# Optimization experiments

Measured on AMD Instinct MI355X. Metric: run time of the kernel, lower is better.

## Reference

```python
import jax, jax.numpy as jnp
import numpy as np

BS, NC, CN, DN = 8, 1024, 64, 64
GH, GW = 32, 32
ALPHA, BPC = 4, 4
G = 8
IN_LO, IN_HI = 0, ALPHA
OUT_LO, OUT_HI = ALPHA, 2 * ALPHA
B_LO, B_HI = 2 * ALPHA, 2 * ALPHA + BPC
HS, HM, HMOD = 256, 256, 128
MOD_IN = 3 * DN + 2 + BPC
MOD_OUT = DN + BPC


def setup_inputs():
    key = jax.random.key(0)
    ks = iter(jax.random.split(key, 40))
    def nrm(shape, s=0.05):
        return jax.random.normal(next(ks), shape, dtype=jnp.float32) * s
    return {
        "x": nrm((BS, NC * DN), 1.0),
        "h": nrm((BS, NC, CN, DN), 0.01),
        "msg": nrm((BS, NC, CN, DN), 0.1),
        "W": nrm((BS, NC, CN, CN), 0.1),
        "decay_logit": jnp.zeros((BS, NC, CN), jnp.float32),
        "cell_context": jnp.zeros((BS, NC, DN), jnp.float32),
        "border_gate_logit": jnp.zeros((BS, NC, BPC), jnp.float32),
        "neuron_id": nrm((NC, CN, DN), 0.02),
        "state_w1": nrm((HS, 2 * DN)), "state_b1": jnp.zeros((HS,), jnp.float32),
        "state_gs1": jnp.ones((G, HS), jnp.float32), "state_gb1": jnp.zeros((G, HS), jnp.float32),
        "state_w2": nrm((DN, HS)), "state_b2": jnp.zeros((DN,), jnp.float32),
        "state_gs2": jnp.ones((G, DN), jnp.float32), "state_gb2": jnp.zeros((G, DN), jnp.float32),
        "msg_w1": nrm((HM, DN)), "msg_b1": jnp.zeros((HM,), jnp.float32),
        "msg_gs1": jnp.ones((G, HM), jnp.float32), "msg_gb1": jnp.zeros((G, HM), jnp.float32),
        "msg_w2": nrm((DN, HM)), "msg_b2": jnp.zeros((DN,), jnp.float32),
        "msg_gs2": jnp.ones((G, DN), jnp.float32), "msg_gb2": jnp.zeros((G, DN), jnp.float32),
        "inject_w": nrm((G, ALPHA * DN, DN)), "inject_b": jnp.zeros((G, ALPHA * DN), jnp.float32),
        "mod_w1": nrm((NC, MOD_IN, HMOD)), "mod_b1": jnp.zeros((NC, HMOD), jnp.float32),
        "mod_w2": nrm((NC, HMOD, MOD_OUT), 0.01), "mod_b2": jnp.zeros((NC, MOD_OUT), jnp.float32),
        "cell_to_group": jnp.arange(NC, dtype=jnp.int32) % G,
    }


def _grouped_mlp(x, c2g, w1, b1, gs1, gb1, w2, b2, gs2, gb2):
    # x: [B, NC, CN, F]; group-specific affine modulation after each linear.
    hid = jnp.einsum('bcnf,hf->bcnh', x, w1) + b1
    hid = jnp.tanh(hid * gs1[c2g][None, :, None, :] + gb1[c2g][None, :, None, :])
    out = jnp.einsum('bcnh,dh->bcnd', hid, w2) + b2
    return jnp.tanh(out * gs2[c2g][None, :, None, :] + gb2[c2g][None, :, None, :])


def reference(x, h, msg, W, decay_logit, cell_context, border_gate_logit, neuron_id,
              state_w1, state_b1, state_gs1, state_gb1, state_w2, state_b2, state_gs2, state_gb2,
              msg_w1, msg_b1, msg_gs1, msg_gb1, msg_w2, msg_b2, msg_gs2, msg_gb2,
              inject_w, inject_b, mod_w1, mod_b1, mod_w2, mod_b2, cell_to_group):
    c2g = cell_to_group
    # 1) dense message passing inside each cell: received = W @ msg
    received = jnp.einsum('bcnm,bcmd->bcnd', W, msg)
    # 2) inject external input into input ports (per-group orthogonal-init projections)
    cell_slice = x.reshape(BS, NC, DN)
    iw, ib = inject_w[c2g], inject_b[c2g]                      # [NC, alpha*DN, DN], [NC, alpha*DN]
    inject = jnp.einsum('bni,noi->bno', cell_slice, iw) + ib   # [BS, NC, alpha*DN]
    received = received.at[:, :, IN_LO:IN_HI].add(inject.reshape(BS, NC, ALPHA, DN))
    # 3) fixed geometric border exchange between neighboring grid cells
    border = msg[:, :, B_LO:B_HI].reshape(BS, GH, GW, BPC, DN)
    incoming = jnp.zeros_like(border)
    incoming = incoming.at[:, 1:, :, 0].set(border[:, :-1, :, 1])
    incoming = incoming.at[:, :-1, :, 1].set(border[:, 1:, :, 0])
    incoming = incoming.at[:, :, 1:, 2].set(border[:, :, :-1, 3])
    incoming = incoming.at[:, :, :-1, 3].set(border[:, :, 1:, 2])
    incoming = incoming.reshape(BS, NC, BPC, DN)
    border_gate = jax.nn.sigmoid(border_gate_logit)[..., None]
    received = received.at[:, :, B_LO:B_HI].add(border_gate * incoming)
    # 4) gated recurrent state update
    decay = jax.nn.sigmoid(decay_logit)[..., None]
    cand = _grouped_mlp(jnp.concatenate([received, h], axis=-1), c2g,
                        state_w1, state_b1, state_gs1, state_gb1,
                        state_w2, state_b2, state_gs2, state_gb2)
    h_new = decay * h + (1.0 - decay) * cand
    # 5) emit new messages (+ per-neuron identity embedding)
    msg_new = _grouped_mlp(h_new, c2g, msg_w1, msg_b1, msg_gs1, msg_gb1,
                           msg_w2, msg_b2, msg_gs2, msg_gb2) + neuron_id[None]
    # 6) readout from output ports
    readout = (msg_new[:, :, OUT_LO:OUT_HI].sum(axis=2) * (ALPHA ** -0.5)).reshape(BS, -1)
    # 7) per-cell modulation MLP (distinct weights per cell)
    h_mean = h_new.mean(axis=2)
    msg_mean = msg_new.mean(axis=2)
    W_row = jnp.abs(W).mean(axis=-1).mean(axis=2, keepdims=True)
    decay_mean = decay_logit.mean(axis=2, keepdims=True)
    feats = jnp.concatenate([h_mean, msg_mean, W_row, decay_mean,
                             cell_context, border_gate_logit], axis=-1)   # [BS, NC, MOD_IN]
    hid = jnp.tanh(jnp.einsum('bcf,cfh->bch', feats, mod_w1) + mod_b1)
    mod = jnp.einsum('bch,cho->bco', hid, mod_w2) + mod_b2                 # [BS, NC, MOD_OUT]
    cell_context_new = cell_context + mod[..., :DN]
    border_gate_logit_new = border_gate_logit + mod[..., DN:]
    return readout, h_new, msg_new, cell_context_new, border_gate_logit_new
```

## Files before the change

### kernel.cpp

```cpp
#include <hip/hip_runtime.h>

#define NCC 1024
#define MODIN 198
#define MODOUT 68
#define HMODL 128

typedef __attribute__((ext_vector_type(8))) short s8v;
typedef __attribute__((ext_vector_type(4))) float f4v;
typedef unsigned short ushort_t;
typedef unsigned int uint_t;

#define OFF_SW1 0
#define OFF_SW2 32768
#define OFF_MW1 49152
#define OFF_MW2 65536
#define FEATS_BYTE_OFF 262144

__device__ __forceinline__ float fast_tanh(float x) {
    const float e = __builtin_amdgcn_exp2f(x * 2.885390081777927f);
    const float r = __builtin_amdgcn_rcpf(e + 1.f);
    return fmaf(-2.f, r, 1.f);
}
__device__ __forceinline__ float fast_sigmoid(float x) {
    const float e = __builtin_amdgcn_exp2f(x * -1.4426950408889634f);
    return __builtin_amdgcn_rcpf(e + 1.f);
}
__device__ __forceinline__ ushort_t f2bf(float x) {
    uint_t u = __builtin_bit_cast(uint_t, x);
    u += 0x7FFFu + ((u >> 16) & 1u);
    return (ushort_t)(u >> 16);
}
__device__ __forceinline__ uint_t pk2(float a, float b) {
    uint_t r;
    asm("v_cvt_pk_bf16_f32 %0, %1, %2" : "=v"(r) : "v"(a), "v"(b));
    return r;
}
#define SWZ(byteoff, row) ((byteoff) ^ (((row) & 7) << 4))

__global__ __launch_bounds__(256)
void mg_cvtw(const float* __restrict__ sw1, const float* __restrict__ sw2,
             const float* __restrict__ mw1, const float* __restrict__ mw2,
             ushort_t* __restrict__ o) {
    const int i = blockIdx.x * 256 + threadIdx.x;
    float v;
    if (i < 32768)      v = sw1[i];
    else if (i < 49152) v = sw2[i - 32768];
    else if (i < 65536) v = mw1[i - 49152];
    else                v = mw2[i - 65536];
    o[i] = f2bf(v);
}

__global__ __launch_bounds__(256, 4)
void mg_inject(const float* __restrict__ xp, const float* __restrict__ iw,
               const float* __restrict__ ibias, const int* __restrict__ c2g,
               float* __restrict__ injb) {
    const int c = blockIdx.x, t = threadIdx.x;
    const int g = c2g[c];
    __shared__ float s_x[8][64];
    for (int idx = t; idx < 512; idx += 256)
        s_x[idx >> 6][idx & 63] = xp[(size_t)(idx >> 6) * (NCC * 64) + c * 64 + (idx & 63)];
    __syncthreads();
    const float* wrow = iw + (size_t)g * 16384 + t * 64;
    float a0 = 0.f, a1 = 0.f, a2 = 0.f, a3 = 0.f, a4 = 0.f, a5 = 0.f, a6 = 0.f, a7 = 0.f;
    #pragma unroll
    for (int i = 0; i < 64; i += 4) {
        const float4 w4 = *(const float4*)(wrow + i);
        const float4 x0 = *(const float4*)&s_x[0][i];
        const float4 x1 = *(const float4*)&s_x[1][i];
        const float4 x2 = *(const float4*)&s_x[2][i];
        const float4 x3 = *(const float4*)&s_x[3][i];
        const float4 x4 = *(const float4*)&s_x[4][i];
        const float4 x5 = *(const float4*)&s_x[5][i];
        const float4 x6 = *(const float4*)&s_x[6][i];
        const float4 x7 = *(const float4*)&s_x[7][i];
        a0 = fmaf(w4.x, x0.x, a0); a0 = fmaf(w4.y, x0.y, a0); a0 = fmaf(w4.z, x0.z, a0); a0 = fmaf(w4.w, x0.w, a0);
        a1 = fmaf(w4.x, x1.x, a1); a1 = fmaf(w4.y, x1.y, a1); a1 = fmaf(w4.z, x1.z, a1); a1 = fmaf(w4.w, x1.w, a1);
        a2 = fmaf(w4.x, x2.x, a2); a2 = fmaf(w4.y, x2.y, a2); a2 = fmaf(w4.z, x2.z, a2); a2 = fmaf(w4.w, x2.w, a2);
        a3 = fmaf(w4.x, x3.x, a3); a3 = fmaf(w4.y, x3.y, a3); a3 = fmaf(w4.z, x3.z, a3); a3 = fmaf(w4.w, x3.w, a3);
        a4 = fmaf(w4.x, x4.x, a4); a4 = fmaf(w4.y, x4.y, a4); a4 = fmaf(w4.z, x4.z, a4); a4 = fmaf(w4.w, x4.w, a4);
        a5 = fmaf(w4.x, x5.x, a5); a5 = fmaf(w4.y, x5.y, a5); a5 = fmaf(w4.z, x5.z, a5); a5 = fmaf(w4.w, x5.w, a5);
        a6 = fmaf(w4.x, x6.x, a6); a6 = fmaf(w4.y, x6.y, a6); a6 = fmaf(w4.z, x6.z, a6); a6 = fmaf(w4.w, x6.w, a6);
        a7 = fmaf(w4.x, x7.x, a7); a7 = fmaf(w4.y, x7.y, a7); a7 = fmaf(w4.z, x7.z, a7); a7 = fmaf(w4.w, x7.w, a7);
    }
    const float bv = ibias[g * 256 + t];
    const float acc[8] = {a0, a1, a2, a3, a4, a5, a6, a7};
    #pragma unroll
    for (int b = 0; b < 8; b++)
        injb[((size_t)b * NCC + c) * 4096 + t] = acc[b] + bv;
}

__global__ __launch_bounds__(512, 4)
void mg_cell_kernel(
    const float* __restrict__ hp,   const float* __restrict__ msgp,
    const float* __restrict__ Wp,   const float* __restrict__ decayp,
    const float* __restrict__ bglp, const float* __restrict__ nidp,
    const float* __restrict__ sb1,  const float* __restrict__ sgs1,
    const float* __restrict__ sgb1, const float* __restrict__ sb2,
    const float* __restrict__ sgs2, const float* __restrict__ sgb2,
    const float* __restrict__ mb1,  const float* __restrict__ mgs1,
    const float* __restrict__ mgb1, const float* __restrict__ mb2,
    const float* __restrict__ mgs2, const float* __restrict__ mgb2,
    const int*   __restrict__ c2g,  const ushort_t* __restrict__ wb,
    float* __restrict__ out_read, float* __restrict__ out_h,
    float* __restrict__ out_msg,  float* __restrict__ wsf)
{
    const int t  = threadIdx.x;
    const int bc = blockIdx.x;
    const int b  = bc >> 10, c = bc & 1023;
    const int gh = c >> 5, gwc = c & 31;
    const int lane = t & 63, w = t >> 6;
    const int cl = lane & 15, q = lane >> 4;
    const int g  = c2g[c];
    const size_t tile = (size_t)bc * 4096;

    __shared__ ushort_t sHid[8192];
    __shared__ ushort_t sIn[8192];
    __shared__ float s_scr[256];
    __shared__ float s_dec[64];
    __shared__ float s_wsum[8];
    __shared__ float s_dsum;

    ushort_t* sW    = sHid;
    ushort_t* sMsgT = sHid + 4096;

    {
        const int n = t >> 3, m0 = (t & 7) * 8;
        const float* src = Wp + tile + n * 64 + m0;
        const float4 v0 = *(const float4*)(src);
        const float4 v1 = *(const float4*)(src + 4);
        float wsum = fabsf(v0.x) + fabsf(v0.y) + fabsf(v0.z) + fabsf(v0.w)
                   + fabsf(v1.x) + fabsf(v1.y) + fabsf(v1.z) + fabsf(v1.w);
        *(uint_t*)((char*)sW + SWZ(n * 128 + (m0 + 0) * 2, n)) = pk2(v0.x, v0.y);
        *(uint_t*)((char*)sW + SWZ(n * 128 + (m0 + 2) * 2, n)) = pk2(v0.z, v0.w);
        *(uint_t*)((char*)sW + SWZ(n * 128 + (m0 + 4) * 2, n)) = pk2(v1.x, v1.y);
        *(uint_t*)((char*)sW + SWZ(n * 128 + (m0 + 6) * 2, n)) = pk2(v1.z, v1.w);
        #pragma unroll
        for (int off = 32; off > 0; off >>= 1) wsum += __shfl_down(wsum, off);
        if (lane == 0) s_wsum[w] = wsum;
    }
    #pragma unroll
    for (int i = 0; i < 2; i++) {
        const int m = (t >> 4) + i * 32, d0 = (t & 15) * 4;
        const float4 v = *(const float4*)(msgp + tile + (size_t)m * 64 + d0);
        *(ushort_t*)((char*)sMsgT + SWZ((d0 + 0) * 128 + m * 2, d0 + 0)) = f2bf(v.x);
        *(ushort_t*)((char*)sMsgT + SWZ((d0 + 1) * 128 + m * 2, d0 + 1)) = f2bf(v.y);
        *(ushort_t*)((char*)sMsgT + SWZ((d0 + 2) * 128 + m * 2, d0 + 2)) = f2bf(v.z);
        *(ushort_t*)((char*)sMsgT + SWZ((d0 + 3) * 128 + m * 2, d0 + 3)) = f2bf(v.w);
    }
    #pragma unroll
    for (int i = 0; i < 2; i++) {
        const int n = (t >> 4) + i * 32, d0 = (t & 15) * 4;
        const float4 v = *(const float4*)(hp + tile + (size_t)n * 64 + d0);
        *(uint_t*)((char*)sIn + SWZ(n * 256 + (64 + d0) * 2, n))     = pk2(v.x, v.y);
        *(uint_t*)((char*)sIn + SWZ(n * 256 + (64 + d0 + 2) * 2, n)) = pk2(v.z, v.w);
    }
    if (t < 256) {
        const int p = w, dd = lane;
        int ok, nc2, qq;
        if      (p == 0) { ok = (gh > 0);   nc2 = c - 32; qq = 1; }
        else if (p == 1) { ok = (gh < 31);  nc2 = c + 32; qq = 0; }
        else if (p == 2) { ok = (gwc > 0);  nc2 = c - 1;  qq = 3; }
        else             { ok = (gwc < 31); nc2 = c + 1;  qq = 2; }
        float v = 0.f;
        if (ok) v = msgp[((size_t)b * NCC + nc2) * 4096 + (8 + qq) * 64 + dd];
        s_scr[p * 64 + dd] = fast_sigmoid(bglp[(size_t)bc * 4 + p]) * v;
    }
    if (w == 4) {
        const float dl = decayp[(size_t)bc * 64 + lane];
        s_dec[lane] = fast_sigmoid(dl);
        float v = dl;
        #pragma unroll
        for (int off = 32; off > 0; off >>= 1) v += __shfl_down(v, off);
        if (lane == 0) s_dsum = v;
    }
    __syncthreads();

    const f4v fzero = {0.f, 0.f, 0.f, 0.f};
    const int d0 = 16 * (w & 3) + q * 4;
    const int dA = 16 * (w & 3) + cl;
    const int rh = w >> 2;

    {
        f4v wm[2] = {fzero, fzero};
        __builtin_amdgcn_s_setprio(1);
        #pragma unroll
        for (int ks = 0; ks < 2; ks++) {
            const int k0 = ks * 32 + q * 8;
            const s8v am = *(const s8v*)((const char*)sMsgT + SWZ(dA * 128 + k0 * 2, dA));
            #pragma unroll
            for (int nt = 0; nt < 2; nt++) {
                const int ar = (rh * 2 + nt) * 16 + cl;
                const s8v bw = *(const s8v*)((const char*)sW + SWZ(ar * 128 + k0 * 2, ar));
                wm[nt] = __builtin_amdgcn_mfma_f32_16x16x32_bf16(am, bw, wm[nt], 0, 0, 0);
            }
        }
        __builtin_amdgcn_s_setprio(0);
        #pragma unroll
        for (int nt = 0; nt < 2; nt++) {
            const int n = (rh * 2 + nt) * 16 + cl;
            float v0 = wm[nt][0], v1 = wm[nt][1], v2 = wm[nt][2], v3 = wm[nt][3];
            if (n < 4) {
                const float4 inj = *(const float4*)(out_h + tile + (size_t)n * 64 + d0);
                v0 += inj.x; v1 += inj.y; v2 += inj.z; v3 += inj.w;
            } else if (n >= 8 && n < 12) {
                const float4 bin = *(const float4*)&s_scr[(n - 8) * 64 + d0];
                v0 += bin.x; v1 += bin.y; v2 += bin.z; v3 += bin.w;
            }
            uint2 pkd; pkd.x = pk2(v0, v1); pkd.y = pk2(v2, v3);
            *(uint2*)((char*)sIn + SWZ(n * 256 + d0 * 2, n)) = pkd;
        }
    }
    __syncthreads();

    {
        f4v a2[2][2];
        a2[0][0] = fzero; a2[0][1] = fzero; a2[1][0] = fzero; a2[1][1] = fzero;
        const ushort_t* wb1 = wb + OFF_SW1;
        const ushort_t* wb2 = wb + OFF_SW2;
        #pragma unroll
        for (int p = 0; p < 2; p++) {
            {
                f4v acc[4] = {fzero, fzero, fzero, fzero};
                const int hrow = p * 128 + 16 * w + cl;
                __builtin_amdgcn_s_setprio(1);
                #pragma unroll
                for (int ks = 0; ks < 4; ks++) {
                    const int k0 = ks * 32 + q * 8;
                    const s8v aw = *(const s8v*)(wb1 + (size_t)hrow * 128 + k0);
                    #pragma unroll
                    for (int rt = 0; rt < 4; rt++) {
                        const int ar = rt * 16 + cl;
                        const s8v bi = *(const s8v*)((const char*)sIn + SWZ(ar * 256 + k0 * 2, ar));
                        acc[rt] = __builtin_amdgcn_mfma_f32_16x16x32_bf16(aw, bi, acc[rt], 0, 0, 0);
                    }
                }
                __builtin_amdgcn_s_setprio(0);
                const int hc0 = p * 128 + 16 * w + q * 4;
                const float4 b1 = *(const float4*)&sb1[hc0];
                const float4 g1 = *(const float4*)&sgs1[g * 256 + hc0];
                const float4 o1 = *(const float4*)&sgb1[g * 256 + hc0];
                const int lc0 = 16 * w + q * 4;
                #pragma unroll
                for (int rt = 0; rt < 4; rt++) {
                    const int n = rt * 16 + cl;
                    const float t0 = fast_tanh(fmaf(acc[rt][0] + b1.x, g1.x, o1.x));
                    const float t1 = fast_tanh(fmaf(acc[rt][1] + b1.y, g1.y, o1.y));
                    const float t2 = fast_tanh(fmaf(acc[rt][2] + b1.z, g1.z, o1.z));
                    const float t3 = fast_tanh(fmaf(acc[rt][3] + b1.w, g1.w, o1.w));
                    uint2 pkd; pkd.x = pk2(t0, t1); pkd.y = pk2(t2, t3);
                    *(uint2*)((char*)sHid + SWZ(n * 256 + lc0 * 2, n)) = pkd;
                }
            }
            __syncthreads();
            {
                __builtin_amdgcn_s_setprio(1);
                #pragma unroll
                for (int ks = 0; ks < 4; ks++) {
                    const int k0 = ks * 32 + q * 8;
                    const s8v aw = *(const s8v*)(wb2 + (size_t)dA * 256 + p * 128 + k0);
                    #pragma unroll
                    for (int nt = 0; nt < 2; nt++) {
                        const int ar = (rh * 2 + nt) * 16 + cl;
                        const s8v bh = *(const s8v*)((const char*)sHid + SWZ(ar * 256 + k0 * 2, ar));
                        a2[nt][ks & 1] = __builtin_amdgcn_mfma_f32_16x16x32_bf16(aw, bh, a2[nt][ks & 1], 0, 0, 0);
                    }
                }
                __builtin_amdgcn_s_setprio(0);
            }
            if (p == 0) __syncthreads();
        }
        const float4 b2 = *(const float4*)&sb2[d0];
        const float4 g2 = *(const float4*)&sgs2[g * 64 + d0];
        const float4 o2 = *(const float4*)&sgb2[g * 64 + d0];
        float hs0 = 0.f, hs1 = 0.f, hs2 = 0.f, hs3 = 0.f;
        #pragma unroll
        for (int nt = 0; nt < 2; nt++) {
            const int n = (rh * 2 + nt) * 16 + cl;
            const float dec = s_dec[n];
            const uint2 hu = *(const uint2*)((const char*)sIn + SWZ(n * 256 + (64 + d0) * 2, n));
            const float hv0 = __builtin_bit_cast(float, (uint_t)(hu.x << 16));
            const float hv1 = __builtin_bit_cast(float, hu.x & 0xFFFF0000u);
            const float hv2 = __builtin_bit_cast(float, (uint_t)(hu.y << 16));
            const float hv3 = __builtin_bit_cast(float, hu.y & 0xFFFF0000u);
            const float c0 = fast_tanh(fmaf(a2[nt][0][0] + a2[nt][1][0] + b2.x, g2.x, o2.x));
            const float c1 = fast_tanh(fmaf(a2[nt][0][1] + a2[nt][1][1] + b2.y, g2.y, o2.y));
            const float c2 = fast_tanh(fmaf(a2[nt][0][2] + a2[nt][1][2] + b2.z, g2.z, o2.z));
            const float c3 = fast_tanh(fmaf(a2[nt][0][3] + a2[nt][1][3] + b2.w, g2.w, o2.w));
            float4 hn;
            hn.x = fmaf(dec, hv0 - c0, c0);
            hn.y = fmaf(dec, hv1 - c1, c1);
            hn.z = fmaf(dec, hv2 - c2, c2);
            hn.w = fmaf(dec, hv3 - c3, c3);
            *(float4*)(out_h + tile + (size_t)n * 64 + d0) = hn;
            uint2 pkd; pkd.x = pk2(hn.x, hn.y); pkd.y = pk2(hn.z, hn.w);
            *(uint2*)((char*)sIn + SWZ(n * 256 + d0 * 2, n)) = pkd;
            hs0 += hn.x; hs1 += hn.y; hs2 += hn.z; hs3 += hn.w;
        }
        #pragma unroll
        for (int m = 1; m < 16; m <<= 1) {
            hs0 += __shfl_xor(hs0, m); hs1 += __shfl_xor(hs1, m);
            hs2 += __shfl_xor(hs2, m); hs3 += __shfl_xor(hs3, m);
        }
        if (cl == 0) {
            float4 hp4 = {hs0, hs1, hs2, hs3};
            *(float4*)&s_scr[rh * 64 + d0] = hp4;
        }
    }
    __syncthreads();

    {
        f4v a6[2][2];
        a6[0][0] = fzero; a6[0][1] = fzero; a6[1][0] = fzero; a6[1][1] = fzero;
        const ushort_t* wm1 = wb + OFF_MW1;
        const ushort_t* wm2 = wb + OFF_MW2;
        #pragma unroll
        for (int p = 0; p < 2; p++) {
            {
                f4v acc[4] = {fzero, fzero, fzero, fzero};
                const int hrow = p * 128 + 16 * w + cl;
                __builtin_amdgcn_s_setprio(1);
                #pragma unroll
                for (int ks = 0; ks < 2; ks++) {
                    const int k0 = ks * 32 + q * 8;
                    const s8v aw = *(const s8v*)(wm1 + (size_t)hrow * 64 + k0);
                    #pragma unroll
                    for (int rt = 0; rt < 4; rt++) {
                        const int ar = rt * 16 + cl;
                        const s8v bi = *(const s8v*)((const char*)sIn + SWZ(ar * 256 + k0 * 2, ar));
                        acc[rt] = __builtin_amdgcn_mfma_f32_16x16x32_bf16(aw, bi, acc[rt], 0, 0, 0);
                    }
                }
                __builtin_amdgcn_s_setprio(0);
                const int hc0 = p * 128 + 16 * w + q * 4;
                const float4 b1 = *(const float4*)&mb1[hc0];
                const float4 g1 = *(const float4*)&mgs1[g * 256 + hc0];
                const float4 o1 = *(const float4*)&mgb1[g * 256 + hc0];
                const int lc0 = 16 * w + q * 4;
                #pragma unroll
                for (int rt = 0; rt < 4; rt++) {
                    const int n = rt * 16 + cl;
                    const float t0 = fast_tanh(fmaf(acc[rt][0] + b1.x, g1.x, o1.x));
                    const float t1 = fast_tanh(fmaf(acc[rt][1] + b1.y, g1.y, o1.y));
                    const float t2 = fast_tanh(fmaf(acc[rt][2] + b1.z, g1.z, o1.z));
                    const float t3 = fast_tanh(fmaf(acc[rt][3] + b1.w, g1.w, o1.w));
                    uint2 pkd; pkd.x = pk2(t0, t1); pkd.y = pk2(t2, t3);
                    *(uint2*)((char*)sHid + SWZ(n * 256 + lc0 * 2, n)) = pkd;
                }
            }
            __syncthreads();
            {
                __builtin_amdgcn_s_setprio(1);
                #pragma unroll
                for (int ks = 0; ks < 4; ks++) {
                    const int k0 = ks * 32 + q * 8;
                    const s8v aw = *(const s8v*)(wm2 + (size_t)dA * 256 + p * 128 + k0);
                    #pragma unroll
                    for (int nt = 0; nt < 2; nt++) {
                        const int ar = (rh * 2 + nt) * 16 + cl;
                        const s8v bh = *(const s8v*)((const char*)sHid + SWZ(ar * 256 + k0 * 2, ar));
                        a6[nt][ks & 1] = __builtin_amdgcn_mfma_f32_16x16x32_bf16(aw, bh, a6[nt][ks & 1], 0, 0, 0);
                    }
                }
                __builtin_amdgcn_s_setprio(0);
            }
            if (p == 0) __syncthreads();
        }
        const float4 b2 = *(const float4*)&mb2[d0];
        const float4 g2 = *(const float4*)&mgs2[g * 64 + d0];
        const float4 o2 = *(const float4*)&mgb2[g * 64 + d0];
        float ms0 = 0.f, ms1 = 0.f, ms2 = 0.f, ms3 = 0.f;
        float ro0 = 0.f, ro1 = 0.f, ro2 = 0.f, ro3 = 0.f;
        #pragma unroll
        for (int nt = 0; nt < 2; nt++) {
            const int n = (rh * 2 + nt) * 16 + cl;
            const float4 nv = *(const float4*)(nidp + (size_t)c * 4096 + (size_t)n * 64 + d0);
            float4 mv;
            mv.x = fast_tanh(fmaf(a6[nt][0][0] + a6[nt][1][0] + b2.x, g2.x, o2.x)) + nv.x;
            mv.y = fast_tanh(fmaf(a6[nt][0][1] + a6[nt][1][1] + b2.y, g2.y, o2.y)) + nv.y;
            mv.z = fast_tanh(fmaf(a6[nt][0][2] + a6[nt][1][2] + b2.z, g2.z, o2.z)) + nv.z;
            mv.w = fast_tanh(fmaf(a6[nt][0][3] + a6[nt][1][3] + b2.w, g2.w, o2.w)) + nv.w;
            *(float4*)(out_msg + tile + (size_t)n * 64 + d0) = mv;
            ms0 += mv.x; ms1 += mv.y; ms2 += mv.z; ms3 += mv.w;
            if (nt == 0 && rh == 0 && n >= 4 && n < 8) {
                ro0 = mv.x; ro1 = mv.y; ro2 = mv.z; ro3 = mv.w;
            }
        }
        #pragma unroll
        for (int m = 1; m < 16; m <<= 1) {
            ms0 += __shfl_xor(ms0, m); ms1 += __shfl_xor(ms1, m);
            ms2 += __shfl_xor(ms2, m); ms3 += __shfl_xor(ms3, m);
        }
        if (cl == 0) {
            float4 mp4 = {ms0, ms1, ms2, ms3};
            *(float4*)&s_scr[128 + rh * 64 + d0] = mp4;
        }
        ro0 += __shfl_xor(ro0, 1); ro1 += __shfl_xor(ro1, 1);
        ro2 += __shfl_xor(ro2, 1); ro3 += __shfl_xor(ro3, 1);
        ro0 += __shfl_xor(ro0, 2); ro1 += __shfl_xor(ro1, 2);
        ro2 += __shfl_xor(ro2, 2); ro3 += __shfl_xor(ro3, 2);
        if (rh == 0 && cl == 4) {
            float4 o4 = {ro0 * 0.5f, ro1 * 0.5f, ro2 * 0.5f, ro3 * 0.5f};
            *(float4*)(out_read + ((size_t)b * NCC + c) * 64 + d0) = o4;
        }
    }
    __syncthreads();

    if (t < 132) {
        float v = 0.f;
        if (t < 64)        v = (s_scr[t] + s_scr[64 + t]) * (1.f / 64.f);
        else if (t < 128)  v = (s_scr[64 + t] + s_scr[128 + t]) * (1.f / 64.f);
        else if (t == 128) v = (s_wsum[0] + s_wsum[1] + s_wsum[2] + s_wsum[3]
                              + s_wsum[4] + s_wsum[5] + s_wsum[6] + s_wsum[7]) * (1.f / 4096.f);
        else if (t == 129) v = s_dsum * (1.f / 64.f);
        wsf[(size_t)bc * 132 + t] = v;
    }
}

__global__ __launch_bounds__(256, 2)
void mg_mod_kernel(
    const float* __restrict__ wsf,   const float* __restrict__ modw1,
    const float* __restrict__ modb1, const float* __restrict__ modw2,
    const float* __restrict__ modb2, const float* __restrict__ ctxp,
    const float* __restrict__ bglp,  float* __restrict__ out_ctx,
    float* __restrict__ out_bg)
{
    const int c = blockIdx.x;
    const int t = threadIdx.x;
    __shared__ float s_f[8][MODIN];
    __shared__ float s_h2[8][HMODL];

    for (int k = t; k < 8 * MODIN; k += 256) {
        const int b = k / MODIN, f = k - b * MODIN;
        float v;
        if (f < 130)      v = wsf[((size_t)b * NCC + c) * 132 + f];
        else if (f < 194) v = ctxp[((size_t)b * NCC + c) * 64 + (f - 130)];
        else              v = bglp[((size_t)b * NCC + c) * 4 + (f - 194)];
        s_f[b][f] = v;
    }
    __syncthreads();

    {
        const int hh = t & 127, bh = (t >> 7) * 4;
        float a0 = 0.f, a1 = 0.f, a2 = 0.f, a3 = 0.f;
        const float* wp = modw1 + (size_t)c * MODIN * HMODL + hh;
        for (int f = 0; f < MODIN; f++) {
            const float wv = wp[(size_t)f * HMODL];
            a0 = fmaf(s_f[bh + 0][f], wv, a0);
            a1 = fmaf(s_f[bh + 1][f], wv, a1);
            a2 = fmaf(s_f[bh + 2][f], wv, a2);
            a3 = fmaf(s_f[bh + 3][f], wv, a3);
        }
        const float bv = modb1[(size_t)c * HMODL + hh];
        s_h2[bh + 0][hh] = fast_tanh(a0 + bv);
        s_h2[bh + 1][hh] = fast_tanh(a1 + bv);
        s_h2[bh + 2][hh] = fast_tanh(a2 + bv);
        s_h2[bh + 3][hh] = fast_tanh(a3 + bv);
    }
    __syncthreads();

    for (int idx = t; idx < 8 * MODOUT; idx += 256) {
        const int b = idx / MODOUT, o = idx - b * MODOUT;
        float acc = modb2[(size_t)c * MODOUT + o];
        const float* wp = modw2 + (size_t)c * HMODL * MODOUT + o;
        const float* hrow = s_h2[b];
        for (int hh = 0; hh < HMODL; hh++)
            acc = fmaf(hrow[hh], wp[(size_t)hh * MODOUT], acc);
        if (o < 64)
            out_ctx[((size_t)b * NCC + c) * 64 + o] =
                ctxp[((size_t)b * NCC + c) * 64 + o] + acc;
        else
            out_bg[((size_t)b * NCC + c) * 4 + (o - 64)] =
                bglp[((size_t)b * NCC + c) * 4 + (o - 64)] + acc;
    }
}

extern "C" void kernel_launch(void* const* d_in, const int* in_sizes, int n_in,
                              void* d_out, int out_size, void* d_ws, size_t ws_size,
                              hipStream_t stream) {
    const float* xp     = (const float*)d_in[0];
    const float* hp     = (const float*)d_in[1];
    const float* msgp   = (const float*)d_in[2];
    const float* Wp     = (const float*)d_in[3];
    const float* decayp = (const float*)d_in[4];
    const float* ctxp   = (const float*)d_in[5];
    const float* bglp   = (const float*)d_in[6];
    const float* nidp   = (const float*)d_in[7];
    const float* sw1    = (const float*)d_in[8];
    const float* sb1    = (const float*)d_in[9];
    const float* sgs1   = (const float*)d_in[10];
    const float* sgb1   = (const float*)d_in[11];
    const float* sw2    = (const float*)d_in[12];
    const float* sb2    = (const float*)d_in[13];
    const float* sgs2   = (const float*)d_in[14];
    const float* sgb2   = (const float*)d_in[15];
    const float* mw1    = (const float*)d_in[16];
    const float* mb1    = (const float*)d_in[17];
    const float* mgs1   = (const float*)d_in[18];
    const float* mgb1   = (const float*)d_in[19];
    const float* mw2    = (const float*)d_in[20];
    const float* mb2    = (const float*)d_in[21];
    const float* mgs2   = (const float*)d_in[22];
    const float* mgb2   = (const float*)d_in[23];
    const float* iw     = (const float*)d_in[24];
    const float* ibias  = (const float*)d_in[25];
    const float* modw1  = (const float*)d_in[26];
    const float* modb1  = (const float*)d_in[27];
    const float* modw2  = (const float*)d_in[28];
    const float* modb2  = (const float*)d_in[29];
    const int*   c2g    = (const int*)d_in[30];

    float* out      = (float*)d_out;
    float* out_read = out;
    float* out_h    = out_read + 524288;
    float* out_msg  = out_h + 33554432;
    float* out_ctx  = out_msg + 33554432;
    float* out_bg   = out_ctx + 524288;

    ushort_t* wb  = (ushort_t*)d_ws;
    float*    wsf = (float*)((char*)d_ws + FEATS_BYTE_OFF);

    mg_cvtw<<<320, 256, 0, stream>>>(sw1, sw2, mw1, mw2, wb);

    mg_inject<<<1024, 256, 0, stream>>>(xp, iw, ibias, c2g, out_h);

    mg_cell_kernel<<<8192, 512, 0, stream>>>(
        hp, msgp, Wp, decayp, bglp, nidp,
        sb1, sgs1, sgb1, sb2, sgs2, sgb2,
        mb1, mgs1, mgb1, mb2, mgs2, mgb2,
        c2g, wb, out_read, out_h, out_msg, wsf);

    mg_mod_kernel<<<1024, 256, 0, stream>>>(
        wsf, modw1, modb1, modw2, modb2, ctxp, bglp, out_ctx, out_bg);
}
```

Baseline: 435.0 us.

## Compute full 256-wide hidden layer in one pass and prefetch next-stage weights

The state and message MLPs used to compute the hidden layer in two 128-column halves, each needing its own sync pair. Each wave now computes 32 hidden columns at once, so the whole 256-wide hidden tile sits in a doubled shared buffer, and the second GEMM runs over K=256 after a single barrier. The first weight fragments for the next GEMM are loaded early (awP0/awP1) to hide global-load latency. This removes several barriers per block but doubles sHid LDS usage and adds accumulator registers, which may reduce occupancy.

```diff
diff --git a/kernel.cpp b/kernel.cpp
--- a/kernel.cpp
+++ b/kernel.cpp
@@ -113,7 +113,7 @@
     const int g  = c2g[c];
     const size_t tile = (size_t)bc * 4096;
 
-    __shared__ ushort_t sHid[8192];
+    __shared__ ushort_t sHid[16384];
     __shared__ ushort_t sIn[8192];
     __shared__ float s_scr[256];
     __shared__ float s_dec[64];
@@ -179,6 +179,12 @@
     const int d0 = 16 * (w & 3) + q * 4;
     const int dA = 16 * (w & 3) + cl;
     const int rh = w >> 2;
+    const ushort_t* wb1 = wb + OFF_SW1;
+    const ushort_t* wb2 = wb + OFF_SW2;
+    const ushort_t* wm1 = wb + OFF_MW1;
+    const ushort_t* wm2 = wb + OFF_MW2;
+
+    s8v awP0, awP1;
 
     {
         f4v wm[2] = {fzero, fzero};
@@ -195,6 +201,8 @@
             }
         }
         __builtin_amdgcn_s_setprio(0);
+        awP0 = *(const s8v*)(wb1 + (size_t)(32 * w + cl) * 128 + q * 8);
+        awP1 = *(const s8v*)(wb1 + (size_t)(32 * w + 16 + cl) * 128 + q * 8);
         #pragma unroll
         for (int nt = 0; nt < 2; nt++) {
             const int n = (rh * 2 + nt) * 16 + cl;
@@ -213,62 +221,69 @@
     __syncthreads();
 
     {
+        f4v acc[2][4];
+        #pragma unroll
+        for (int i = 0; i < 2; i++)
+            #pragma unroll
+            for (int j = 0; j < 4; j++) acc[i][j] = fzero;
+        __builtin_amdgcn_s_setprio(1);
+        #pragma unroll
+        for (int ks = 0; ks < 4; ks++) {
+            const int k0 = ks * 32 + q * 8;
+            const s8v aw0 = (ks == 0) ? awP0
+                : *(const s8v*)(wb1 + (size_t)(32 * w + cl) * 128 + k0);
+            const s8v aw1 = (ks == 0) ? awP1
+                : *(const s8v*)(wb1 + (size_t)(32 * w + 16 + cl) * 128 + k0);
+            #pragma unroll
+            for (int rt = 0; rt < 4; rt++) {
+                const int ar = rt * 16 + cl;
+                const s8v bi = *(const s8v*)((const char*)sIn + SWZ(ar * 256 + k0 * 2, ar));
+                acc[0][rt] = __builtin_amdgcn_mfma_f32_16x16x32_bf16(aw0, bi, acc[0][rt], 0, 0, 0);
+                acc[1][rt] = __builtin_amdgcn_mfma_f32_16x16x32_bf16(aw1, bi, acc[1][rt], 0, 0, 0);
+            }
+        }
+        __builtin_amdgcn_s_setprio(0);
+        awP0 = *(const s8v*)(wb2 + (size_t)dA * 256 + q * 8);
+        awP1 = *(const s8v*)(wb2 + (size_t)dA * 256 + 32 + q * 8);
+        #pragma unroll
+        for (int ct = 0; ct < 2; ct++) {
+            const int hc0 = 32 * w + ct * 16 + q * 4;
+            const float4 b1 = *(const float4*)&sb1[hc0];
+            const float4 g1 = *(const float4*)&sgs1[g * 256 + hc0];
+            const float4 o1 = *(const float4*)&sgb1[g * 256 + hc0];
+            #pragma unroll
+            for (int rt = 0; rt < 4; rt++) {
+                const int n = rt * 16 + cl;
+                const float t0 = fast_tanh(fmaf(acc[ct][rt][0] + b1.x, g1.x, o1.x));
+                const float t1 = fast_tanh(fmaf(acc[ct][rt][1] + b1.y, g1.y, o1.y));
+                const float t2 = fast_tanh(fmaf(acc[ct][rt][2] + b1.z, g1.z, o1.z));
+                const float t3 = fast_tanh(fmaf(acc[ct][rt][3] + b1.w, g1.w, o1.w));
+                uint2 pkd; pkd.x = pk2(t0, t1); pkd.y = pk2(t2, t3);
+                *(uint2*)((char*)sHid + SWZ(n * 512 + hc0 * 2, n)) = pkd;
+            }
+        }
+    }
+    __syncthreads();
+
+    {
         f4v a2[2][2];
         a2[0][0] = fzero; a2[0][1] = fzero; a2[1][0] = fzero; a2[1][1] = fzero;
-        const ushort_t* wb1 = wb + OFF_SW1;
-        const ushort_t* wb2 = wb + OFF_SW2;
-        #pragma unroll
-        for (int p = 0; p < 2; p++) {
-            {
-                f4v acc[4] = {fzero, fzero, fzero, fzero};
-                const int hrow = p * 128 + 16 * w + cl;
-                __builtin_amdgcn_s_setprio(1);
-                #pragma unroll
-                for (int ks = 0; ks < 4; ks++) {
-                    const int k0 = ks * 32 + q * 8;
-                    const s8v aw = *(const s8v*)(wb1 + (size_t)hrow * 128 + k0);
-                    #pragma unroll
-                    for (int rt = 0; rt < 4; rt++) {
-                        const int ar = rt * 16 + cl;
-                        const s8v bi = *(const s8v*)((const char*)sIn + SWZ(ar * 256 + k0 * 2, ar));
-                        acc[rt] = __builtin_amdgcn_mfma_f32_16x16x32_bf16(aw, bi, acc[rt], 0, 0, 0);
-                    }
-                }
-                __builtin_amdgcn_s_setprio(0);
-                const int hc0 = p * 128 + 16 * w + q * 4;
-                const float4 b1 = *(const float4*)&sb1[hc0];
-                const float4 g1 = *(const float4*)&sgs1[g * 256 + hc0];
-                const float4 o1 = *(const float4*)&sgb1[g * 256 + hc0];
-                const int lc0 = 16 * w + q * 4;
-                #pragma unroll
-                for (int rt = 0; rt < 4; rt++) {
-                    const int n = rt * 16 + cl;
-                    const float t0 = fast_tanh(fmaf(acc[rt][0] + b1.x, g1.x, o1.x));
-                    const float t1 = fast_tanh(fmaf(acc[rt][1] + b1.y, g1.y, o1.y));
-                    const float t2 = fast_tanh(fmaf(acc[rt][2] + b1.z, g1.z, o1.z));
-                    const float t3 = fast_tanh(fmaf(acc[rt][3] + b1.w, g1.w, o1.w));
-                    uint2 pkd; pkd.x = pk2(t0, t1); pkd.y = pk2(t2, t3);
-                    *(uint2*)((char*)sHid + SWZ(n * 256 + lc0 * 2, n)) = pkd;
-                }
-            }
-            __syncthreads();
-            {
-                __builtin_amdgcn_s_setprio(1);
-                #pragma unroll
-                for (int ks = 0; ks < 4; ks++) {
-                    const int k0 = ks * 32 + q * 8;
-                    const s8v aw = *(const s8v*)(wb2 + (size_t)dA * 256 + p * 128 + k0);
-                    #pragma unroll
-                    for (int nt = 0; nt < 2; nt++) {
-                        const int ar = (rh * 2 + nt) * 16 + cl;
-                        const s8v bh = *(const s8v*)((const char*)sHid + SWZ(ar * 256 + k0 * 2, ar));
-                        a2[nt][ks & 1] = __builtin_amdgcn_mfma_f32_16x16x32_bf16(aw, bh, a2[nt][ks & 1], 0, 0, 0);
-                    }
-                }
-                __builtin_amdgcn_s_setprio(0);
-            }
-            if (p == 0) __syncthreads();
-        }
+        __builtin_amdgcn_s_setprio(1);
+        #pragma unroll
+        for (int ks = 0; ks < 8; ks++) {
+            const int k0 = ks * 32 + q * 8;
+            const s8v aw = (ks == 0) ? awP0 : (ks == 1) ? awP1
+                : *(const s8v*)(wb2 + (size_t)dA * 256 + k0);
+            #pragma unroll
+            for (int nt = 0; nt < 2; nt++) {
+                const int ar = (rh * 2 + nt) * 16 + cl;
+                const s8v bh = *(const s8v*)((const char*)sHid + SWZ(ar * 512 + k0 * 2, ar));
+                a2[nt][ks & 1] = __builtin_amdgcn_mfma_f32_16x16x32_bf16(aw, bh, a2[nt][ks & 1], 0, 0, 0);
+            }
+        }
+        __builtin_amdgcn_s_setprio(0);
+        awP0 = *(const s8v*)(wm1 + (size_t)(32 * w + cl) * 64 + q * 8);
+        awP1 = *(const s8v*)(wm1 + (size_t)(32 * w + 16 + cl) * 64 + q * 8);
         const float4 b2 = *(const float4*)&sb2[d0];
         const float4 g2 = *(const float4*)&sgs2[g * 64 + d0];
         const float4 o2 = *(const float4*)&sgb2[g * 64 + d0];
@@ -309,62 +324,67 @@
     __syncthreads();
 
     {
+        f4v acc[2][4];
+        #pragma unroll
+        for (int i = 0; i < 2; i++)
+            #pragma unroll
+            for (int j = 0; j < 4; j++) acc[i][j] = fzero;
+        __builtin_amdgcn_s_setprio(1);
+        #pragma unroll
+        for (int ks = 0; ks < 2; ks++) {
+            const int k0 = ks * 32 + q * 8;
+            const s8v aw0 = (ks == 0) ? awP0
+                : *(const s8v*)(wm1 + (size_t)(32 * w + cl) * 64 + k0);
+            const s8v aw1 = (ks == 0) ? awP1
+                : *(const s8v*)(wm1 + (size_t)(32 * w + 16 + cl) * 64 + k0);
+            #pragma unroll
+            for (int rt = 0; rt < 4; rt++) {
+                const int ar = rt * 16 + cl;
+                const s8v bi = *(const s8v*)((const char*)sIn + SWZ(ar * 256 + k0 * 2, ar));
+                acc[0][rt] = __builtin_amdgcn_mfma_f32_16x16x32_bf16(aw0, bi, acc[0][rt], 0, 0, 0);
+                acc[1][rt] = __builtin_amdgcn_mfma_f32_16x16x32_bf16(aw1, bi, acc[1][rt], 0, 0, 0);
+            }
+        }
+        __builtin_amdgcn_s_setprio(0);
+        awP0 = *(const s8v*)(wm2 + (size_t)dA * 256 + q * 8);
+        awP1 = *(const s8v*)(wm2 + (size_t)dA * 256 + 32 + q * 8);
+        #pragma unroll
+        for (int ct = 0; ct < 2; ct++) {
+            const int hc0 = 32 * w + ct * 16 + q * 4;
+            const float4 b1 = *(const float4*)&mb1[hc0];
+            const float4 g1 = *(const float4*)&mgs1[g * 256 + hc0];
+            const float4 o1 = *(const float4*)&mgb1[g * 256 + hc0];
+            #pragma unroll
+            for (int rt = 0; rt < 4; rt++) {
+                const int n = rt * 16 + cl;
+                const float t0 = fast_tanh(fmaf(acc[ct][rt][0] + b1.x, g1.x, o1.x));
+                const float t1 = fast_tanh(fmaf(acc[ct][rt][1] + b1.y, g1.y, o1.y));
+                const float t2 = fast_tanh(fmaf(acc[ct][rt][2] + b1.z, g1.z, o1.z));
+                const float t3 = fast_tanh(fmaf(acc[ct][rt][3] + b1.w, g1.w, o1.w));
+                uint2 pkd; pkd.x = pk2(t0, t1); pkd.y = pk2(t2, t3);
+                *(uint2*)((char*)sHid + SWZ(n * 512 + hc0 * 2, n)) = pkd;
+            }
+        }
+    }
+    __syncthreads();
+
+    {
         f4v a6[2][2];
         a6[0][0] = fzero; a6[0][1] = fzero; a6[1][0] = fzero; a6[1][1] = fzero;
-        const ushort_t* wm1 = wb + OFF_MW1;
-        const ushort_t* wm2 = wb + OFF_MW2;
-        #pragma unroll
-        for (int p = 0; p < 2; p++) {
-            {
-                f4v acc[4] = {fzero, fzero, fzero, fzero};
-                const int hrow = p * 128 + 16 * w + cl;
-                __builtin_amdgcn_s_setprio(1);
-                #pragma unroll
-                for (int ks = 0; ks < 2; ks++) {
-                    const int k0 = ks * 32 + q * 8;
-                    const s8v aw = *(const s8v*)(wm1 + (size_t)hrow * 64 + k0);
-                    #pragma unroll
-                    for (int rt = 0; rt < 4; rt++) {
-                        const int ar = rt * 16 + cl;
-                        const s8v bi = *(const s8v*)((const char*)sIn + SWZ(ar * 256 + k0 * 2, ar));
-                        acc[rt] = __builtin_amdgcn_mfma_f32_16x16x32_bf16(aw, bi, acc[rt], 0, 0, 0);
-                    }
-                }
-                __builtin_amdgcn_s_setprio(0);
-                const int hc0 = p * 128 + 16 * w + q * 4;
-                const float4 b1 = *(const float4*)&mb1[hc0];
-                const float4 g1 = *(const float4*)&mgs1[g * 256 + hc0];
-                const float4 o1 = *(const float4*)&mgb1[g * 256 + hc0];
-                const int lc0 = 16 * w + q * 4;
-                #pragma unroll
-                for (int rt = 0; rt < 4; rt++) {
-                    const int n = rt * 16 + cl;
-                    const float t0 = fast_tanh(fmaf(acc[rt][0] + b1.x, g1.x, o1.x));
-                    const float t1 = fast_tanh(fmaf(acc[rt][1] + b1.y, g1.y, o1.y));
-                    const float t2 = fast_tanh(fmaf(acc[rt][2] + b1.z, g1.z, o1.z));
-                    const float t3 = fast_tanh(fmaf(acc[rt][3] + b1.w, g1.w, o1.w));
-                    uint2 pkd; pkd.x = pk2(t0, t1); pkd.y = pk2(t2, t3);
-                    *(uint2*)((char*)sHid + SWZ(n * 256 + lc0 * 2, n)) = pkd;
-                }
-            }
-            __syncthreads();
-            {
-                __builtin_amdgcn_s_setprio(1);
-                #pragma unroll
-                for (int ks = 0; ks < 4; ks++) {
-                    const int k0 = ks * 32 + q * 8;
-                    const s8v aw = *(const s8v*)(wm2 + (size_t)dA * 256 + p * 128 + k0);
-                    #pragma unroll
-                    for (int nt = 0; nt < 2; nt++) {
-                        const int ar = (rh * 2 + nt) * 16 + cl;
-                        const s8v bh = *(const s8v*)((const char*)sHid + SWZ(ar * 256 + k0 * 2, ar));
-                        a6[nt][ks & 1] = __builtin_amdgcn_mfma_f32_16x16x32_bf16(aw, bh, a6[nt][ks & 1], 0, 0, 0);
-                    }
-                }
-                __builtin_amdgcn_s_setprio(0);
-            }
-            if (p == 0) __syncthreads();
-        }
+        __builtin_amdgcn_s_setprio(1);
+        #pragma unroll
+        for (int ks = 0; ks < 8; ks++) {
+            const int k0 = ks * 32 + q * 8;
+            const s8v aw = (ks == 0) ? awP0 : (ks == 1) ? awP1
+                : *(const s8v*)(wm2 + (size_t)dA * 256 + k0);
+            #pragma unroll
+            for (int nt = 0; nt < 2; nt++) {
+                const int ar = (rh * 2 + nt) * 16 + cl;
+                const s8v bh = *(const s8v*)((const char*)sHid + SWZ(ar * 512 + k0 * 2, ar));
+                a6[nt][ks & 1] = __builtin_amdgcn_mfma_f32_16x16x32_bf16(aw, bh, a6[nt][ks & 1], 0, 0, 0);
+            }
+        }
+        __builtin_amdgcn_s_setprio(0);
         const float4 b2 = *(const float4*)&mb2[d0];
         const float4 g2 = *(const float4*)&mgs2[g * 64 + d0];
         const float4 o2 = *(const float4*)&mgb2[g * 64 + d0];
```

After: 394.8 us (median of 2 runs). 9.3% less time.
